# Kernel tuning notes

Measured on AMD Instinct MI355X. Metric: run time of the kernel, lower is better.

The kernel has to match this reference:

```python
import jax, jax.numpy as jnp
import numpy as np

B, T, C, H = 4, 4096, 512, 64

def setup_inputs() -> dict:
    key = jax.random.key(0)
    ks = jax.random.split(key, 9)
    k = jax.random.normal(ks[0], (B, T, C), dtype=jnp.float32)
    v = jax.random.normal(ks[1], (B, T, C), dtype=jnp.float32)
    q = jax.random.normal(ks[2], (B, T, C), dtype=jnp.float32)
    # causal lower-triangular mask, positions with 0 are masked to -inf
    mask = jnp.tril(jnp.ones((T, T), dtype=jnp.int32))
    s = 1.0 / np.sqrt(C)
    kW = jax.random.normal(ks[3], (C, H), dtype=jnp.float32) * s
    kb = jax.random.normal(ks[4], (H,), dtype=jnp.float32) * s
    vW = jax.random.normal(ks[5], (C, H), dtype=jnp.float32) * s
    vb = jax.random.normal(ks[6], (H,), dtype=jnp.float32) * s
    qW = jax.random.normal(ks[7], (C, H), dtype=jnp.float32) * s
    qb = jax.random.normal(ks[8], (H,), dtype=jnp.float32) * s
    return {"k": k, "v": v, "q": q, "mask": mask,
            "kW": kW, "kb": kb, "vW": vW, "vb": vb, "qW": qW, "qb": qb}

def reference(k, v, q, mask, kW, kb, vW, vb, qW, qb):
    C_in = k.shape[-1]
    kp = k @ kW + kb                              # [B,T,H]
    qp = q @ qW + qb                              # [B,T,H]
    # NOTE: original scales by embedding_size**-0.5 (C), not head_size**-0.5
    attn = jnp.einsum('bth,bsh->bts', qp, kp) * (C_in ** -0.5)  # [B,T,T]
    attn = jnp.where(mask[None, :, :] == 0, -jnp.inf, attn)
    attn = jax.nn.softmax(attn, axis=-1)
    vp = v @ vW + vb                              # [B,T,H]
    out = attn @ vp                               # [B,T,H]
    return out
```

## Files before the change

kernel.cpp:

```cpp
#include <hip/hip_runtime.h>
#include <hip/hip_bf16.h>

#define Bq 4
#define Tq 4096
#define Cq 512
#define Hq 64
#define NEG_BIG (-3.0e38f)

using bf16   = __bf16;
using bf16x8 = __attribute__((ext_vector_type(8))) __bf16;
using bf16x4 = __attribute__((ext_vector_type(4))) __bf16;
using f32x4  = __attribute__((ext_vector_type(4))) float;
using f32x16 = __attribute__((ext_vector_type(16))) float;

static __device__ __forceinline__ float other_half_f(float x) {
    return __shfl_xor(x, 32, 64);
}
static __device__ __forceinline__ unsigned other_half_u(unsigned x) {
    return (unsigned)__shfl_xor((int)x, 32, 64);
}
static __device__ __forceinline__ unsigned pk2(float x, float y) {
    union { bf16 h[2]; unsigned u; } t;
    t.h[0] = (bf16)x; t.h[1] = (bf16)y;
    return t.u;
}
union W8 { unsigned u[4]; bf16x8 v; };

#define BUILD_B(p, BA, BB) do {                                                \
    const unsigned w0 = pk2(p[0],  p[1]),  w1 = pk2(p[2],  p[3]);              \
    const unsigned w2 = pk2(p[4],  p[5]),  w3 = pk2(p[6],  p[7]);              \
    const unsigned w4 = pk2(p[8],  p[9]),  w5 = pk2(p[10], p[11]);             \
    const unsigned w6 = pk2(p[12], p[13]), w7 = pk2(p[14], p[15]);             \
    const unsigned o0 = other_half_u(w0), o1 = other_half_u(w1);               \
    const unsigned o2 = other_half_u(w2), o3 = other_half_u(w3);               \
    const unsigned o4 = other_half_u(w4), o5 = other_half_u(w5);               \
    const unsigned o6 = other_half_u(w6), o7 = other_half_u(w7);               \
    BA.u[0] = hi ? o2 : w0;  BA.u[1] = hi ? o3 : w1;                           \
    BA.u[2] = hi ? w2 : o0;  BA.u[3] = hi ? w3 : o1;                           \
    BB.u[0] = hi ? o6 : w4;  BB.u[1] = hi ? o7 : w5;                           \
    BB.u[2] = hi ? w6 : o4;  BB.u[3] = hi ? w7 : o5;                           \
} while (0)

__global__ __launch_bounds__(256) void prep_weights_kernel(
    const float* __restrict__ kW, const float* __restrict__ qW,
    const float* __restrict__ vW, bf16* __restrict__ WT)
{
    int i = blockIdx.x * 256 + threadIdx.x;
    int t = i >> 15;
    int r = i & 32767;
    int c = r >> 6;
    int h = r & 63;
    const float* W = (t == 0) ? kW : (t == 1) ? qW : vW;
    WT[(size_t)t * 32768 + h * 512 + c] = (bf16)W[r];
}

__global__ __launch_bounds__(256, 2) void proj_kernel(
    const float* __restrict__ Xk, const float* __restrict__ Xq,
    const float* __restrict__ Xv, const bf16* __restrict__ WT,
    const float* __restrict__ bk, const float* __restrict__ bq,
    const float* __restrict__ bv,
    bf16* __restrict__ kp, bf16* __restrict__ qp, bf16* __restrict__ vpT)
{
    __shared__ float Xs[2][64 * 128];

    const int t = blockIdx.y;
    const float* X    = (t == 0) ? Xk : (t == 1) ? Xq : Xv;
    const float* bias = (t == 0) ? bk : (t == 1) ? bq : bv;
    const bf16*  Wt   = WT + (size_t)t * (Hq * Cq);

    const int tid  = threadIdx.x;
    const int wave = tid >> 6;
    const int lane = tid & 63;
    const int lq   = lane & 15;
    const int lg   = lane >> 4;
    const int r0   = blockIdx.x * 64;
    const float* Xb = X + (size_t)r0 * Cq;

#define STAGE(BUF, STEP) do {                                                  \
    const int kc_ = (STEP) * 128;                                              \
    _Pragma("unroll")                                                          \
    for (int j = 0; j < 8; ++j) {                                              \
        const int i2   = wave * 8 + j;                                         \
        const int rloc = 2 * i2 + (lane >> 5);                                 \
        const int scol = (lane & 31) ^ (rloc & 7);                             \
        const float* src_ = Xb + (size_t)rloc * Cq + kc_ + scol * 4;           \
        __builtin_amdgcn_global_load_lds(                                      \
            (const __attribute__((address_space(1))) void*)(src_),             \
            (__attribute__((address_space(3))) void*)(&Xs[BUF][i2 * 256]),     \
            16, 0, 0);                                                         \
    }                                                                          \
} while (0)

    f32x4 acc[4];
#pragma unroll
    for (int i = 0; i < 4; ++i) acc[i] = f32x4{0.f, 0.f, 0.f, 0.f};

    STAGE(0, 0);
    __syncthreads();

    const int rloc_c = wave * 16 + lq;
    const int sw     = lq & 7;

#pragma unroll
    for (int s = 0; s < 4; ++s) {
        if (s < 3) STAGE((s + 1) & 1, s + 1);
        const float* lb = &Xs[s & 1][0] + (size_t)rloc_c * 128;

#pragma unroll
        for (int ch = 0; ch < 4; ++ch) {
            const int c = ch * 8 + lg * 2;
            const float4 x0 = *(const float4*)(lb + ((c ^ sw) * 4));
            const float4 x1 = *(const float4*)(lb + (((c + 1) ^ sw) * 4));
            bf16x8 af;
            af[0] = (bf16)x0.x; af[1] = (bf16)x0.y;
            af[2] = (bf16)x0.z; af[3] = (bf16)x0.w;
            af[4] = (bf16)x1.x; af[5] = (bf16)x1.y;
            af[6] = (bf16)x1.z; af[7] = (bf16)x1.w;
            const int kg = s * 128 + ch * 32;
#pragma unroll
            for (int ht = 0; ht < 4; ++ht) {
                bf16x8 bfB = *(const bf16x8*)(Wt + (size_t)(ht * 16 + lq) * Cq + kg + lg * 8);
                acc[ht] = __builtin_amdgcn_mfma_f32_16x16x32_bf16(af, bfB, acc[ht], 0, 0, 0);
            }
        }
        __syncthreads();
    }
#undef STAGE

    const float scale = (t == 1) ? (0.044194173824159216f * 1.4426950408889634f) : 1.0f;
    const int row0 = r0 + wave * 16;

    if (t < 2) {
        bf16* dst = (t == 0) ? kp : qp;
#pragma unroll
        for (int ht = 0; ht < 4; ++ht) {
            float bb = bias[ht * 16 + lq];
#pragma unroll
            for (int r = 0; r < 4; ++r) {
                int row = row0 + 4 * lg + r;
                dst[(size_t)row * Hq + ht * 16 + lq] = (bf16)((acc[ht][r] + bb) * scale);
            }
        }
    } else {
#pragma unroll
        for (int ht = 0; ht < 4; ++ht) {
            float bb = bias[ht * 16 + lq];
            bf16x4 pk;
#pragma unroll
            for (int r = 0; r < 4; ++r) pk[r] = (bf16)(acc[ht][r] + bb);
            int rowg = row0 + 4 * lg;
            int bidx = rowg >> 12;
            int tt   = rowg & 4095;
            int h    = ht * 16 + lq;
            *(bf16x4*)(vpT + (((size_t)(bidx * Hq + h)) << 12) + tt) = pk;
        }
    }
}

__global__ __launch_bounds__(256, 2) void attn_kernel(
    const bf16* __restrict__ qp, const bf16* __restrict__ kp,
    const bf16* __restrict__ vpT,
    bf16* __restrict__ PO, float* __restrict__ PML)
{
    __shared__ char lds_raw[2][16384];

    const int x = blockIdx.x;
    const int b = x & 3;
    const int j = 31 - ((x >> 2) & 31);
    const int c = x >> 7;
    const int kstart = c * 512;
    const int klim   = (j + 1) * 128;
    if (kstart >= klim) return;
    const int kend = min(kstart + 512, klim);
    const int nt   = (kend - kstart) >> 6;

    const int tid  = threadIdx.x;
    const int wid  = tid >> 6;
    const int lane = tid & 63;
    const int l31  = lane & 31;
    const int half = lane >> 5;
    const bool hi  = half != 0;
    const int qt   = j * 4 + wid;
    const int qb   = qt * 32;
    const int qg   = qb + l31;
    const int qlast = qb + 31;

    const bf16* kp_b = kp  + (size_t)b * Tq * Hq;
    const bf16* vp_b = vpT + (size_t)b * Hq * Tq;

    const int srow = tid >> 2;
    const int sseg = (tid & 3) * 16;
    const int sswz = (srow & 7) << 4;

#define STAGE_LOAD(T, r0, r1, r2, r3) do {                                     \
    const int k0_ = kstart + (T) * 64;                                         \
    const bf16* kg_ = kp_b + (size_t)(k0_ + srow) * Hq + (sseg >> 1);          \
    r0 = *(const int4*)(kg_);                                                  \
    r1 = *(const int4*)(kg_ + 32);                                             \
    const bf16* vg_ = vp_b + (size_t)srow * Tq + k0_ + (sseg >> 1);            \
    r2 = *(const int4*)(vg_);                                                  \
    r3 = *(const int4*)(vg_ + 32);                                             \
} while (0)

#define STAGE_WRITE(BUF, r0, r1, r2, r3) do {                                  \
    char* base_ = lds_raw[BUF];                                                \
    *(int4*)(base_ + srow * 128 + (sseg ^ sswz))          = r0;                \
    *(int4*)(base_ + srow * 128 + ((sseg + 64) ^ sswz))   = r1;                \
    *(int4*)(base_ + 8192 + srow * 128 + (sseg ^ sswz))        = r2;           \
    *(int4*)(base_ + 8192 + srow * 128 + ((sseg + 64) ^ sswz)) = r3;           \
} while (0)

    const bf16* qrow = qp + ((size_t)b * Tq + qb + l31) * Hq + half * 8;
    const bf16x8 Q0 = *(const bf16x8*)(qrow);
    const bf16x8 Q1 = *(const bf16x8*)(qrow + 16);
    const bf16x8 Q2 = *(const bf16x8*)(qrow + 32);
    const bf16x8 Q3 = *(const bf16x8*)(qrow + 48);

    f32x16 O0, O1;
#pragma unroll
    for (int r = 0; r < 16; ++r) { O0[r] = 0.f; O1[r] = 0.f; }
    float l = 0.f;

    const int rswz = (l31 & 7) << 4;
    const int cb   = half * 16;

    int4 s0, s1, s2, s3;
    STAGE_LOAD(0, s0, s1, s2, s3);
    STAGE_WRITE(0, s0, s1, s2, s3);
    __syncthreads();

    int cur = 0;
    for (int t = 0; t < nt; ++t) {
        const bool more = (t + 1 < nt);
        if (more) STAGE_LOAD(t + 1, s0, s1, s2, s3);

        const int k0t = kstart + t * 64;
        if (k0t <= qlast) {
            const char* base = lds_raw[cur];
            const char* kr0 = base + l31 * 128;
            const char* kr1 = base + (32 + l31) * 128;
            const char* vr0 = base + 8192 + l31 * 128;
            const char* vr1 = base + 8192 + (32 + l31) * 128;

            const bf16x8 K00 = *(const bf16x8*)(kr0 + ((cb +  0) ^ rswz));
            const bf16x8 K01 = *(const bf16x8*)(kr0 + ((cb + 32) ^ rswz));
            const bf16x8 K02 = *(const bf16x8*)(kr0 + ((cb + 64) ^ rswz));
            const bf16x8 K03 = *(const bf16x8*)(kr0 + ((cb + 96) ^ rswz));
            const bf16x8 K10 = *(const bf16x8*)(kr1 + ((cb +  0) ^ rswz));
            const bf16x8 K11 = *(const bf16x8*)(kr1 + ((cb + 32) ^ rswz));
            const bf16x8 K12 = *(const bf16x8*)(kr1 + ((cb + 64) ^ rswz));
            const bf16x8 K13 = *(const bf16x8*)(kr1 + ((cb + 96) ^ rswz));
            const bf16x8 Vh0k0 = *(const bf16x8*)(vr0 + ((cb +  0) ^ rswz));
            const bf16x8 Vh0k1 = *(const bf16x8*)(vr0 + ((cb + 32) ^ rswz));
            const bf16x8 Vh0k2 = *(const bf16x8*)(vr0 + ((cb + 64) ^ rswz));
            const bf16x8 Vh0k3 = *(const bf16x8*)(vr0 + ((cb + 96) ^ rswz));
            const bf16x8 Vh1k0 = *(const bf16x8*)(vr1 + ((cb +  0) ^ rswz));
            const bf16x8 Vh1k1 = *(const bf16x8*)(vr1 + ((cb + 32) ^ rswz));
            const bf16x8 Vh1k2 = *(const bf16x8*)(vr1 + ((cb + 64) ^ rswz));
            const bf16x8 Vh1k3 = *(const bf16x8*)(vr1 + ((cb + 96) ^ rswz));

            f32x16 S0, S1;
#pragma unroll
            for (int r = 0; r < 16; ++r) { S0[r] = 0.f; S1[r] = 0.f; }
            S0 = __builtin_amdgcn_mfma_f32_32x32x16_bf16(K00, Q0, S0, 0, 0, 0);
            S1 = __builtin_amdgcn_mfma_f32_32x32x16_bf16(K10, Q0, S1, 0, 0, 0);
            S0 = __builtin_amdgcn_mfma_f32_32x32x16_bf16(K01, Q1, S0, 0, 0, 0);
            S1 = __builtin_amdgcn_mfma_f32_32x32x16_bf16(K11, Q1, S1, 0, 0, 0);
            S0 = __builtin_amdgcn_mfma_f32_32x32x16_bf16(K02, Q2, S0, 0, 0, 0);
            S1 = __builtin_amdgcn_mfma_f32_32x32x16_bf16(K12, Q2, S1, 0, 0, 0);
            S0 = __builtin_amdgcn_mfma_f32_32x32x16_bf16(K03, Q3, S0, 0, 0, 0);
            S1 = __builtin_amdgcn_mfma_f32_32x32x16_bf16(K13, Q3, S1, 0, 0, 0);

            if (k0t + 63 > qb) {
#pragma unroll
                for (int r = 0; r < 16; ++r) {
                    const int kg = k0t + (r & 3) + 8 * (r >> 2) + 4 * half;
                    if (kg > qg)      S0[r] = NEG_BIG;
                    if (kg + 32 > qg) S1[r] = NEG_BIG;
                }
            }

            float p0[16], p1[16];
#pragma unroll
            for (int r = 0; r < 16; ++r) {
                p0[r] = exp2f(S0[r]);
                p1[r] = exp2f(S1[r]);
            }
            l += (((p0[0]+p0[1])+(p0[2]+p0[3])) + ((p0[4]+p0[5])+(p0[6]+p0[7])))
               + (((p0[8]+p0[9])+(p0[10]+p0[11])) + ((p0[12]+p0[13])+(p0[14]+p0[15])))
               + (((p1[0]+p1[1])+(p1[2]+p1[3])) + ((p1[4]+p1[5])+(p1[6]+p1[7])))
               + (((p1[8]+p1[9])+(p1[10]+p1[11])) + ((p1[12]+p1[13])+(p1[14]+p1[15])));

            W8 B00, B01, B10, B11;
            BUILD_B(p0, B00, B01);
            BUILD_B(p1, B10, B11);

            O0 = __builtin_amdgcn_mfma_f32_32x32x16_bf16(Vh0k0, B00.v, O0, 0, 0, 0);
            O1 = __builtin_amdgcn_mfma_f32_32x32x16_bf16(Vh1k0, B00.v, O1, 0, 0, 0);
            O0 = __builtin_amdgcn_mfma_f32_32x32x16_bf16(Vh0k1, B01.v, O0, 0, 0, 0);
            O1 = __builtin_amdgcn_mfma_f32_32x32x16_bf16(Vh1k1, B01.v, O1, 0, 0, 0);
            O0 = __builtin_amdgcn_mfma_f32_32x32x16_bf16(Vh0k2, B10.v, O0, 0, 0, 0);
            O1 = __builtin_amdgcn_mfma_f32_32x32x16_bf16(Vh1k2, B10.v, O1, 0, 0, 0);
            O0 = __builtin_amdgcn_mfma_f32_32x32x16_bf16(Vh0k3, B11.v, O0, 0, 0, 0);
            O1 = __builtin_amdgcn_mfma_f32_32x32x16_bf16(Vh1k3, B11.v, O1, 0, 0, 0);
        }

        __syncthreads();
        if (more) STAGE_WRITE(cur ^ 1, s0, s1, s2, s3);
        __syncthreads();
        cur ^= 1;
    }
#undef STAGE_LOAD
#undef STAGE_WRITE

    const float ltot = l + other_half_f(l);
    const float inv  = (ltot > 0.f) ? (1.0f / ltot) : 0.f;
    const size_t slot = ((size_t)(b * 128 + qt)) * 8 + c;
    bf16* po = PO + slot * 2048;
#pragma unroll
    for (int r = 0; r < 16; ++r) {
        const int h = (r & 3) + 8 * (r >> 2) + 4 * half;
        po[h * 32 + l31]        = (bf16)(O0[r] * inv);
        po[(h + 32) * 32 + l31] = (bf16)(O1[r] * inv);
    }
    if (lane < 32) {
        PML[slot * 32 + l31] = ltot;
    }
}

__global__ __launch_bounds__(256) void combine_kernel(
    const bf16* __restrict__ PO, const float* __restrict__ PML,
    float* __restrict__ out)
{
    const int gid = blockIdx.x;
    const int b   = gid & 3;
    const int qt  = gid >> 2;
    const int qb  = qt * 32;
    const int nch = ((qt >> 2) + 4) >> 2;
    const size_t slot0 = ((size_t)(b * 128 + qt)) * 8;
    const int tid = threadIdx.x;
    const int q   = tid & 31;
    const int hh  = tid >> 5;

    float L = 0.f;
    float acc[8];
#pragma unroll
    for (int i = 0; i < 8; ++i) acc[i] = 0.f;

    for (int c = 0; c < nch; ++c) {
        const float w = PML[(slot0 + c) * 32 + q];
        L += w;
        const bf16* po = PO + (slot0 + c) * 2048;
#pragma unroll
        for (int ih = 0; ih < 8; ++ih)
            acc[ih] += w * (float)po[(hh + 8 * ih) * 32 + q];
    }
    const float inv = 1.0f / L;
#pragma unroll
    for (int ih = 0; ih < 8; ++ih)
        out[((size_t)b * Tq + qb + q) * Hq + hh + 8 * ih] = acc[ih] * inv;
}

extern "C" void kernel_launch(void* const* d_in, const int* in_sizes, int n_in,
                              void* d_out, int out_size, void* d_ws, size_t ws_size,
                              hipStream_t stream)
{
    const float* k  = (const float*)d_in[0];
    const float* v  = (const float*)d_in[1];
    const float* q  = (const float*)d_in[2];
    const float* kW = (const float*)d_in[4];
    const float* kb = (const float*)d_in[5];
    const float* vW = (const float*)d_in[6];
    const float* vb = (const float*)d_in[7];
    const float* qW = (const float*)d_in[8];
    const float* qb = (const float*)d_in[9];
    float* out = (float*)d_out;

    char* ws = (char*)d_ws;
    bf16*  WT  = (bf16*)(ws);
    bf16*  kp  = (bf16*)(ws + 196608);
    bf16*  qp  = (bf16*)(ws + 196608 + 2097152);
    bf16*  vpT = (bf16*)(ws + 196608 + 2 * 2097152);
    bf16*  PO  = (bf16*)(ws + 196608 + 3 * 2097152);
    float* PML = (float*)(ws + 196608 + 3 * 2097152 + 16777216);

    hipLaunchKernelGGL(prep_weights_kernel, dim3(384), dim3(256), 0, stream,
                       kW, qW, vW, WT);
    hipLaunchKernelGGL(proj_kernel, dim3(256, 3), dim3(256), 0, stream,
                       k, q, v, WT, kb, qb, vb, kp, qp, vpT);
    hipLaunchKernelGGL(attn_kernel, dim3(1024), dim3(256), 0, stream,
                       qp, kp, vpT, PO, PML);
    hipLaunchKernelGGL(combine_kernel, dim3(512), dim3(256), 0, stream,
                       PO, PML, out);
}
```

Measured before the change: 82.66 us.

## Load full-K row tile once in proj kernel with smaller 128-thread blocks

The projection kernel now stages each block's whole 32x512 input slice into LDS with a single barrier, replacing the four-step double-buffered K pipeline. Blocks shrink to 2 waves covering 32 rows, and the grid doubles to 512x3 so more blocks are in flight. This removes per-step barriers and keeps more independent loads outstanding at once. The cost is 64KB of LDS per block, which limits blocks per CU, and there is no longer any overlap of loads with MFMA inside a block.

```diff
diff --git a/kernel.cpp b/kernel.cpp
--- a/kernel.cpp
+++ b/kernel.cpp
@@ -54,14 +54,14 @@
     WT[(size_t)t * 32768 + h * 512 + c] = (bf16)W[r];
 }
 
-__global__ __launch_bounds__(256, 2) void proj_kernel(
+__global__ __launch_bounds__(128) void proj_kernel(
     const float* __restrict__ Xk, const float* __restrict__ Xq,
     const float* __restrict__ Xv, const bf16* __restrict__ WT,
     const float* __restrict__ bk, const float* __restrict__ bq,
     const float* __restrict__ bv,
     bf16* __restrict__ kp, bf16* __restrict__ qp, bf16* __restrict__ vpT)
 {
-    __shared__ float Xs[2][64 * 128];
+    __shared__ float Xs[32 * 512];
 
     const int t = blockIdx.y;
     const float* X    = (t == 0) ? Xk : (t == 1) ? Xq : Xv;
@@ -73,59 +73,49 @@
     const int lane = tid & 63;
     const int lq   = lane & 15;
     const int lg   = lane >> 4;
-    const int r0   = blockIdx.x * 64;
+    const int r0   = blockIdx.x * 32;
     const float* Xb = X + (size_t)r0 * Cq;
 
-#define STAGE(BUF, STEP) do {                                                  \
-    const int kc_ = (STEP) * 128;                                              \
-    _Pragma("unroll")                                                          \
-    for (int j = 0; j < 8; ++j) {                                              \
-        const int i2   = wave * 8 + j;                                         \
-        const int rloc = 2 * i2 + (lane >> 5);                                 \
-        const int scol = (lane & 31) ^ (rloc & 7);                             \
-        const float* src_ = Xb + (size_t)rloc * Cq + kc_ + scol * 4;           \
-        __builtin_amdgcn_global_load_lds(                                      \
-            (const __attribute__((address_space(1))) void*)(src_),             \
-            (__attribute__((address_space(3))) void*)(&Xs[BUF][i2 * 256]),     \
-            16, 0, 0);                                                         \
-    }                                                                          \
-} while (0)
+#pragma unroll
+    for (int j = 0; j < 32; ++j) {
+        const int i  = wave * 32 + j;
+        const int r  = i >> 1;
+        const int h  = i & 1;
+        const int sc = lane ^ (r & 7);
+        const float* src_ = Xb + (size_t)r * Cq + h * 256 + sc * 4;
+        __builtin_amdgcn_global_load_lds(
+            (const __attribute__((address_space(1))) void*)(src_),
+            (__attribute__((address_space(3))) void*)(Xs + i * 256),
+            16, 0, 0);
+    }
+    __syncthreads();
 
     f32x4 acc[4];
 #pragma unroll
     for (int i = 0; i < 4; ++i) acc[i] = f32x4{0.f, 0.f, 0.f, 0.f};
 
-    STAGE(0, 0);
-    __syncthreads();
-
-    const int rloc_c = wave * 16 + lq;
-    const int sw     = lq & 7;
-
-#pragma unroll
-    for (int s = 0; s < 4; ++s) {
-        if (s < 3) STAGE((s + 1) & 1, s + 1);
-        const float* lb = &Xs[s & 1][0] + (size_t)rloc_c * 128;
-
-#pragma unroll
-        for (int ch = 0; ch < 4; ++ch) {
-            const int c = ch * 8 + lg * 2;
-            const float4 x0 = *(const float4*)(lb + ((c ^ sw) * 4));
-            const float4 x1 = *(const float4*)(lb + (((c + 1) ^ sw) * 4));
-            bf16x8 af;
-            af[0] = (bf16)x0.x; af[1] = (bf16)x0.y;
-            af[2] = (bf16)x0.z; af[3] = (bf16)x0.w;
-            af[4] = (bf16)x1.x; af[5] = (bf16)x1.y;
-            af[6] = (bf16)x1.z; af[7] = (bf16)x1.w;
-            const int kg = s * 128 + ch * 32;
-#pragma unroll
-            for (int ht = 0; ht < 4; ++ht) {
-                bf16x8 bfB = *(const bf16x8*)(Wt + (size_t)(ht * 16 + lq) * Cq + kg + lg * 8);
-                acc[ht] = __builtin_amdgcn_mfma_f32_16x16x32_bf16(af, bfB, acc[ht], 0, 0, 0);
-            }
+    const int rl = wave * 16 + lq;
+    const int rx = rl & 7;
+    const float* lb = Xs + (size_t)rl * 512;
+
+#pragma unroll
+    for (int ch = 0; ch < 16; ++ch) {
+        const int h  = ch >> 3;
+        const int sA = (ch & 7) * 8 + lg * 2;
+        const float4 x0 = *(const float4*)(lb + h * 256 + ((sA ^ rx) * 4));
+        const float4 x1 = *(const float4*)(lb + h * 256 + (((sA + 1) ^ rx) * 4));
+        bf16x8 af;
+        af[0] = (bf16)x0.x; af[1] = (bf16)x0.y;
+        af[2] = (bf16)x0.z; af[3] = (bf16)x0.w;
+        af[4] = (bf16)x1.x; af[5] = (bf16)x1.y;
+        af[6] = (bf16)x1.z; af[7] = (bf16)x1.w;
+        const int kg = ch * 32;
+#pragma unroll
+        for (int ht = 0; ht < 4; ++ht) {
+            bf16x8 bfB = *(const bf16x8*)(Wt + (size_t)(ht * 16 + lq) * Cq + kg + lg * 8);
+            acc[ht] = __builtin_amdgcn_mfma_f32_16x16x32_bf16(af, bfB, acc[ht], 0, 0, 0);
         }
-        __syncthreads();
-    }
-#undef STAGE
+    }
 
     const float scale = (t == 1) ? (0.044194173824159216f * 1.4426950408889634f) : 1.0f;
     const int row0 = r0 + wave * 16;
@@ -386,7 +376,7 @@
 
     hipLaunchKernelGGL(prep_weights_kernel, dim3(384), dim3(256), 0, stream,
                        kW, qW, vW, WT);
-    hipLaunchKernelGGL(proj_kernel, dim3(256, 3), dim3(256), 0, stream,
+    hipLaunchKernelGGL(proj_kernel, dim3(512, 3), dim3(128), 0, stream,
                        k, q, v, WT, kb, qb, vb, kp, qp, vpT);
     hipLaunchKernelGGL(attn_kernel, dim3(1024), dim3(256), 0, stream,
                        qp, kp, vpT, PO, PML);
```

After: 86.55 us. 4.7% more time.
